# Performance work log

Measured on AMD Instinct MI355X. Metric: run time of the kernel, lower is better.

Reference implementation:

```python
import jax, jax.numpy as jnp
import numpy as np

EMB = 128
N_LEFT = 100000
N_RIGHT = 100000
N_EDGES = 600000
EDGE_FEAT = 1


def _ortho(key, shape):
    a = jax.random.normal(key, shape, dtype=jnp.float32)
    q, r = jnp.linalg.qr(a if shape[0] >= shape[1] else a.T)
    q = q * jnp.sign(jnp.diag(r))
    return q if shape[0] >= shape[1] else q.T


def setup_inputs() -> dict:
    key = jax.random.key(0)
    ks = jax.random.split(key, 12)
    return {
        "left_features": jax.random.normal(ks[0], (N_LEFT, EMB), dtype=jnp.float32),
        "edge_indices": jax.random.randint(ks[1], (2, N_EDGES), 0, N_LEFT, dtype=jnp.int32).astype(jnp.int64),
        "edge_features": jax.random.normal(ks[2], (N_EDGES, EDGE_FEAT), dtype=jnp.float32),
        "right_features": jax.random.normal(ks[3], (N_RIGHT, EMB), dtype=jnp.float32),
        "scatter_out_size": N_RIGHT,
        # parameters (orthogonal weights, zero biases, unit PreNorm scales)
        "W_left": _ortho(ks[4], (EMB, EMB)),
        "b_left": jnp.zeros((EMB,), jnp.float32),
        "W_edge": _ortho(ks[5], (EMB, EDGE_FEAT)),
        "W_right": _ortho(ks[6], (EMB, EMB)),
        "scale_final": jnp.ones((1,), jnp.float32),
        "W_final": _ortho(ks[7], (EMB, EMB)),
        "b_final": jnp.zeros((EMB,), jnp.float32),
        "scale_post": jnp.ones((1,), jnp.float32),
        "W_out1": _ortho(ks[8], (EMB, 2 * EMB)),
        "b_out1": jnp.zeros((EMB,), jnp.float32),
        "W_out2": _ortho(ks[9], (EMB, EMB)),
        "b_out2": jnp.zeros((EMB,), jnp.float32),
    }


def reference(left_features, edge_indices, edge_features, right_features,
              scatter_out_size, W_left, b_left, W_edge, W_right,
              scale_final, W_final, b_final, scale_post,
              W_out1, b_out1, W_out2, b_out2):
    # node / edge projections
    left_proj = left_features @ W_left.T + b_left            # [n_left, emb]
    edge_proj = edge_features @ W_edge.T                     # [n_edges, emb]
    right_proj = right_features @ W_right.T                  # [n_right, emb]
    # gather per-edge messages and combine
    joint = left_proj[edge_indices[0]] + edge_proj + right_proj[edge_indices[1]]
    # feature_module_final: PreNorm(scale only) -> ReLU -> Linear
    joint = jax.nn.relu(joint * scale_final) @ W_final.T + b_final
    # scatter-add onto right-side nodes (right_to_left=False)
    conv = jax.ops.segment_sum(joint, edge_indices[1], num_segments=scatter_out_size)
    conv = conv * scale_post
    # output MLP on [conv ; prev_right]
    h = jnp.concatenate([conv, right_features], axis=1)      # [n_right, 2*emb]
    h = jax.nn.relu(h @ W_out1.T + b_out1)
    return h @ W_out2.T + b_out2
```

## Files before the change

kernel.cpp:

```cpp
#include <hip/hip_runtime.h>

#define EMB 128

typedef __attribute__((ext_vector_type(8))) short short8;
typedef __attribute__((ext_vector_type(4))) short short4v;
typedef __attribute__((ext_vector_type(4))) float floatx4;

#define MFMA(a, b, c) __builtin_amdgcn_mfma_f32_16x16x32_bf16((a), (b), (c), 0, 0, 0)

__device__ __forceinline__ ushort f2b(float f) {
    unsigned u = __float_as_uint(f);
    return (ushort)((u + 0x7fff + ((u >> 16) & 1)) >> 16);
}
__device__ __forceinline__ float b2f(ushort h) {
    return __uint_as_float(((unsigned)h) << 16);
}
__device__ __forceinline__ short8 cvt8(const float* p) {
    float4 f0 = *(const float4*)p;
    float4 f1 = *(const float4*)(p + 4);
    short8 v;
    v[0] = f2b(f0.x); v[1] = f2b(f0.y); v[2] = f2b(f0.z); v[3] = f2b(f0.w);
    v[4] = f2b(f1.x); v[5] = f2b(f1.y); v[6] = f2b(f1.z); v[7] = f2b(f1.w);
    return v;
}

template <int RSH>
__device__ __forceinline__ void stage32k(const ushort* __restrict__ g,
                                         ushort* __restrict__ lds, int t) {
#pragma unroll
    for (int i = 0; i < 8; i++) {
        int a = i * 4096 + t * 16;
        short8 v = *(const short8*)(g + (a >> 1));
        int d = a ^ (((a >> RSH) & 7) << 4);
        *(short8*)((char*)lds + d) = v;
    }
}
__device__ __forceinline__ short8 ldsW8(const ushort* lds, int byte) {
    return *(const short8*)((const char*)lds + (byte ^ (((byte >> 8) & 7) << 4)));
}
__device__ __forceinline__ short8 ldsW9(const ushort* lds, int byte) {
    return *(const short8*)((const char*)lds + (byte ^ (((byte >> 9) & 7) << 4)));
}

__global__ __launch_bounds__(256) void k_cvthist(const float* __restrict__ w0,
                                                 const float* __restrict__ w1,
                                                 const float* __restrict__ w2,
                                                 const float* __restrict__ w3,
                                                 const float* __restrict__ w4,
                                                 ushort* __restrict__ dst,
                                                 const int* __restrict__ eidx,
                                                 int* __restrict__ cnt,
                                                 int n_edges) {
    int bid = blockIdx.x;
    if (bid < 384) {
        int i = bid * 256 + threadIdx.x;
        const float* src; int off;
        if (i < 16384)      { src = w0; off = i; }
        else if (i < 32768) { src = w1; off = i - 16384; }
        else if (i < 49152) { src = w2; off = i - 32768; }
        else if (i < 81920) { src = w3; off = i - 49152; }
        else                { src = w4; off = i - 81920; }
        dst[i] = f2b(src[off]);
    } else {
        int e = (bid - 384) * 256 + threadIdx.x;
        if (e < n_edges) atomicAdd(&cnt[eidx[n_edges + e]], 1);
    }
}

#define SCAN_CHUNK 4096
__global__ __launch_bounds__(1024) void k_scan1(const int* __restrict__ cnt,
                                                int* __restrict__ offs,
                                                int* __restrict__ bsum, int n) {
    __shared__ int buf[1024];
    int t = threadIdx.x;
    int i0 = blockIdx.x * SCAN_CHUNK + t * 4;
    int v[4];
#pragma unroll
    for (int u = 0; u < 4; u++) { int i = i0 + u; v[u] = (i < n) ? cnt[i] : 0; }
    int s = v[0] + v[1] + v[2] + v[3];
    buf[t] = s;
    __syncthreads();
    for (int d = 1; d < 1024; d <<= 1) {
        int x = (t >= d) ? buf[t - d] : 0;
        __syncthreads();
        buf[t] += x;
        __syncthreads();
    }
    int excl = buf[t] - s;
#pragma unroll
    for (int u = 0; u < 4; u++) { int i = i0 + u; if (i < n) offs[i] = excl; excl += v[u]; }
    if (t == 1023) bsum[blockIdx.x] = buf[1023];
}

__global__ __launch_bounds__(1024) void k_scan2(const int* __restrict__ bsum,
                                                int* __restrict__ offs,
                                                int* __restrict__ cursor, int n) {
    int bid = blockIdx.x;
    int base = 0;
    for (int j = 0; j < bid; j++) base += bsum[j];
    int i0 = bid * SCAN_CHUNK + threadIdx.x * 4;
#pragma unroll
    for (int u = 0; u < 4; u++) {
        int i = i0 + u;
        if (i < n) { int o = offs[i] + base; offs[i] = o; cursor[i] = o; }
    }
}

#define PROJ_PB 512
__global__ __launch_bounds__(256) void k_permproj(const int* __restrict__ eidx,
                                                  const float* __restrict__ ef,
                                                  int* __restrict__ cursor,
                                                  int2* __restrict__ sle,
                                                  int n_edges,
                                                  const float* __restrict__ XL,
                                                  const float* __restrict__ XR,
                                                  const ushort* __restrict__ WLb,
                                                  const ushort* __restrict__ WRb,
                                                  const float* __restrict__ bias,
                                                  ushort* __restrict__ YL,
                                                  ushort* __restrict__ YR,
                                                  int n, int eb) {
    __shared__ ushort Wlds[16384];
    int bid = blockIdx.x;
    if (bid < eb) {
        int e = bid * 256 + threadIdx.x;
        if (e < n_edges) {
            int r = eidx[n_edges + e];
            int p = atomicAdd(&cursor[r], 1);
            int2 v; v.x = eidx[e]; v.y = __float_as_int(ef[e]);
            sle[p] = v;
        }
        return;
    }
    bid -= eb;
    const float* X; const ushort* Wb; ushort* Y; int has_bias;
    if (bid < PROJ_PB) { X = XL; Wb = WLb; Y = YL; has_bias = 1; }
    else               { X = XR; Wb = WRb; Y = YR; has_bias = 0; bid -= PROJ_PB; }

    int t = threadIdx.x, wave = t >> 6, lane = t & 63;
    int m = lane & 15, quad = lane >> 4;

    stage32k<8>(Wb, Wlds, t);
    __syncthreads();

    int ntiles = (n + 127) >> 7;
    for (int tile = bid; tile < ntiles; tile += PROJ_PB) {
        size_t base = (size_t)tile * 128 + wave * 32;
        size_t ra = base + m;
        size_t rb = base + 16 + m;
        bool oka = ra < (size_t)n, okb = rb < (size_t)n;
        size_t rac = oka ? ra : (size_t)(n - 1);
        size_t rbc = okb ? rb : (size_t)(n - 1);
        const float* pa = X + rac * EMB;
        const float* pb = X + rbc * EMB;
        short8 xa[4], xb[4];
#pragma unroll
        for (int ks = 0; ks < 4; ks++) {
            xa[ks] = cvt8(pa + ks * 32 + quad * 8);
            xb[ks] = cvt8(pb + ks * 32 + quad * 8);
        }
#pragma unroll
        for (int wt = 0; wt < 8; wt++) {
            floatx4 a0 = {0.f, 0.f, 0.f, 0.f}, a1 = {0.f, 0.f, 0.f, 0.f};
#pragma unroll
            for (int ks = 0; ks < 4; ks++) {
                short8 w = ldsW8(Wlds, ((wt * 16 + m) << 8) + (ks << 6) + (quad << 4));
                a0 = MFMA(w, xa[ks], a0);
                a1 = MFMA(w, xb[ks], a1);
            }
            float b0 = 0.f, b1_ = 0.f, b2_ = 0.f, b3 = 0.f;
            if (has_bias) {
                float4 bb = *(const float4*)(bias + wt * 16 + quad * 4);
                b0 = bb.x; b1_ = bb.y; b2_ = bb.z; b3 = bb.w;
            }
            if (oka) {
                short4v o;
                o[0] = f2b(a0[0] + b0);
                o[1] = f2b(a0[1] + b1_);
                o[2] = f2b(a0[2] + b2_);
                o[3] = f2b(a0[3] + b3);
                *(short4v*)(Y + ra * EMB + wt * 16 + quad * 4) = o;
            }
            if (okb) {
                short4v o;
                o[0] = f2b(a1[0] + b0);
                o[1] = f2b(a1[1] + b1_);
                o[2] = f2b(a1[2] + b2_);
                o[3] = f2b(a1[3] + b3);
                *(short4v*)(Y + rb * EMB + wt * 16 + quad * 4) = o;
            }
        }
    }
}

__global__ __launch_bounds__(256) void k_reduce(const ushort* __restrict__ Pl,
                                                const ushort* __restrict__ Pr,
                                                const int2* __restrict__ sle,
                                                const float* __restrict__ We,
                                                const int* __restrict__ offs,
                                                const float* __restrict__ scale_final,
                                                ushort* __restrict__ S,
                                                int n_right, int n_edges) {
    int r = blockIdx.x * 4 + (threadIdx.x >> 6);
    if (r >= n_right) return;
    int lane = threadIdx.x & 63;
    int g = lane >> 4;
    int m = lane & 15;
    float scale = scale_final[0];

    float4 w0 = *(const float4*)(We + m * 8);
    float4 w1 = *(const float4*)(We + m * 8 + 4);
    short8 prv = *(const short8*)(Pr + (size_t)r * EMB + m * 8);
    float we[8], pr[8];
    we[0] = w0.x; we[1] = w0.y; we[2] = w0.z; we[3] = w0.w;
    we[4] = w1.x; we[5] = w1.y; we[6] = w1.z; we[7] = w1.w;
#pragma unroll
    for (int j = 0; j < 8; j++) pr[j] = b2f((ushort)prv[j]);

    float acc[8] = {0.f, 0.f, 0.f, 0.f, 0.f, 0.f, 0.f, 0.f};
    int s0 = offs[r];
    int s1 = (r + 1 < n_right) ? offs[r + 1] : n_edges;
    int e = s0 + g;
    for (; e + 4 < s1; e += 8) {
        int2 ea = sle[e];
        int2 eb = sle[e + 4];
        short8 pa = *(const short8*)(Pl + (size_t)ea.x * EMB + m * 8);
        short8 pb = *(const short8*)(Pl + (size_t)eb.x * EMB + m * 8);
        float fa = __int_as_float(ea.y), fb = __int_as_float(eb.y);
#pragma unroll
        for (int j = 0; j < 8; j++) {
            acc[j] += fmaxf((b2f((ushort)pa[j]) + pr[j] + fa * we[j]) * scale, 0.f);
            acc[j] += fmaxf((b2f((ushort)pb[j]) + pr[j] + fb * we[j]) * scale, 0.f);
        }
    }
    if (e < s1) {
        int2 ea = sle[e];
        short8 pa = *(const short8*)(Pl + (size_t)ea.x * EMB + m * 8);
        float fa = __int_as_float(ea.y);
#pragma unroll
        for (int j = 0; j < 8; j++)
            acc[j] += fmaxf((b2f((ushort)pa[j]) + pr[j] + fa * we[j]) * scale, 0.f);
    }
#pragma unroll
    for (int j = 0; j < 8; j++) {
        acc[j] += __shfl_xor(acc[j], 16);
        acc[j] += __shfl_xor(acc[j], 32);
    }
    if (g == 0) {
        short8 o;
#pragma unroll
        for (int j = 0; j < 8; j++) o[j] = f2b(acc[j]);
        *(short8*)(S + (size_t)r * EMB + m * 8) = o;
    }
}

__global__ __launch_bounds__(256) void k_out(const ushort* __restrict__ S,
                                             const float* __restrict__ right,
                                             const ushort* __restrict__ Wfb,
                                             const float* __restrict__ bf,
                                             const int* __restrict__ deg,
                                             const float* __restrict__ sc_post,
                                             const ushort* __restrict__ W1b,
                                             const float* __restrict__ b1,
                                             const ushort* __restrict__ W2b,
                                             const float* __restrict__ b2,
                                             float* __restrict__ out, int n) {
    __shared__ ushort Wlds[16384];
    __shared__ ushort H[64][136];
    __shared__ float degs[64];
    int t = threadIdx.x, wave = t >> 6, lane = t & 63;
    int m = lane & 15, quad = lane >> 4;
    size_t row0 = (size_t)blockIdx.x * 64;
    int rl = wave * 16 + m;
    size_t xrow = row0 + rl;
    size_t xrowc = (xrow < (size_t)n) ? xrow : (size_t)(n - 1);
    bool ok = (xrow < (size_t)n);
    float sp = sc_post[0];

    short8 s4[4], ar[4];
    const ushort* sr = S + xrowc * EMB;
    const float* rr = right + xrowc * EMB;
#pragma unroll
    for (int ks = 0; ks < 4; ks++)
        s4[ks] = *(const short8*)(sr + ks * 32 + quad * 8);
    stage32k<8>(Wfb, Wlds, t);
#pragma unroll
    for (int ks = 0; ks < 4; ks++)
        ar[ks] = cvt8(rr + ks * 32 + quad * 8);
    if (t < 64) {
        size_t rr2 = row0 + t;
        degs[t] = (rr2 < (size_t)n) ? (float)deg[rr2] : 0.f;
    }
    __syncthreads();
    float dd = degs[rl];

#pragma unroll
    for (int wt = 0; wt < 8; wt++) {
        floatx4 acc = {0.f, 0.f, 0.f, 0.f};
#pragma unroll
        for (int ks = 0; ks < 4; ks++) {
            short8 w = ldsW8(Wlds, ((wt * 16 + m) << 8) + (ks << 6) + (quad << 4));
            acc = MFMA(w, s4[ks], acc);
        }
        float4 bb = *(const float4*)(bf + wt * 16 + quad * 4);
        short4v o;
        o[0] = f2b((acc[0] + dd * bb.x) * sp);
        o[1] = f2b((acc[1] + dd * bb.y) * sp);
        o[2] = f2b((acc[2] + dd * bb.z) * sp);
        o[3] = f2b((acc[3] + dd * bb.w) * sp);
        *(short4v*)(&H[rl][wt * 16 + quad * 4]) = o;
    }
    short8 c4[4];
#pragma unroll
    for (int ks = 0; ks < 4; ks++)
        c4[ks] = *(const short8*)(&H[rl][ks * 32 + quad * 8]);
    __syncthreads();
    stage32k<9>(W1b, Wlds, t);
    __syncthreads();

#pragma unroll
    for (int wt = 0; wt < 4; wt++) {
        floatx4 acc = {0.f, 0.f, 0.f, 0.f};
        int rb = wt * 16 + m;
#pragma unroll
        for (int ks = 0; ks < 4; ks++) {
            short8 w = ldsW9(Wlds, (rb << 9) + (ks << 6) + (quad << 4));
            acc = MFMA(w, c4[ks], acc);
        }
#pragma unroll
        for (int ks = 0; ks < 4; ks++) {
            short8 w = ldsW9(Wlds, (rb << 9) + 256 + (ks << 6) + (quad << 4));
            acc = MFMA(w, ar[ks], acc);
        }
        float4 bb = *(const float4*)(b1 + wt * 16 + quad * 4);
        short4v o;
        o[0] = f2b(fmaxf(acc[0] + bb.x, 0.f));
        o[1] = f2b(fmaxf(acc[1] + bb.y, 0.f));
        o[2] = f2b(fmaxf(acc[2] + bb.z, 0.f));
        o[3] = f2b(fmaxf(acc[3] + bb.w, 0.f));
        *(short4v*)(&H[rl][wt * 16 + quad * 4]) = o;
    }
    __syncthreads();
    stage32k<9>(W1b + 16384, Wlds, t);
    __syncthreads();

#pragma unroll
    for (int wt = 4; wt < 8; wt++) {
        floatx4 acc = {0.f, 0.f, 0.f, 0.f};
        int rb = (wt - 4) * 16 + m;
#pragma unroll
        for (int ks = 0; ks < 4; ks++) {
            short8 w = ldsW9(Wlds, (rb << 9) + (ks << 6) + (quad << 4));
            acc = MFMA(w, c4[ks], acc);
        }
#pragma unroll
        for (int ks = 0; ks < 4; ks++) {
            short8 w = ldsW9(Wlds, (rb << 9) + 256 + (ks << 6) + (quad << 4));
            acc = MFMA(w, ar[ks], acc);
        }
        float4 bb = *(const float4*)(b1 + wt * 16 + quad * 4);
        short4v o;
        o[0] = f2b(fmaxf(acc[0] + bb.x, 0.f));
        o[1] = f2b(fmaxf(acc[1] + bb.y, 0.f));
        o[2] = f2b(fmaxf(acc[2] + bb.z, 0.f));
        o[3] = f2b(fmaxf(acc[3] + bb.w, 0.f));
        *(short4v*)(&H[rl][wt * 16 + quad * 4]) = o;
    }
    short8 h4[4];
#pragma unroll
    for (int ks = 0; ks < 4; ks++)
        h4[ks] = *(const short8*)(&H[rl][ks * 32 + quad * 8]);
    __syncthreads();
    stage32k<8>(W2b, Wlds, t);
    __syncthreads();

#pragma unroll
    for (int wt = 0; wt < 8; wt++) {
        floatx4 acc = {0.f, 0.f, 0.f, 0.f};
#pragma unroll
        for (int ks = 0; ks < 4; ks++) {
            short8 w = ldsW8(Wlds, ((wt * 16 + m) << 8) + (ks << 6) + (quad << 4));
            acc = MFMA(w, h4[ks], acc);
        }
        if (ok) {
            float4 bb = *(const float4*)(b2 + wt * 16 + quad * 4);
            float4 o;
            o.x = acc[0] + bb.x;
            o.y = acc[1] + bb.y;
            o.z = acc[2] + bb.z;
            o.w = acc[3] + bb.w;
            *(float4*)(out + xrow * EMB + wt * 16 + quad * 4) = o;
        }
    }
}

extern "C" void kernel_launch(void* const* d_in, const int* in_sizes, int n_in,
                              void* d_out, int out_size, void* d_ws, size_t ws_size,
                              hipStream_t stream) {
    const float* left   = (const float*)d_in[0];
    const int*   eidx   = (const int*)  d_in[1];
    const float* efeat  = (const float*)d_in[2];
    const float* right  = (const float*)d_in[3];
    const float* W_left = (const float*)d_in[5];
    const float* b_left = (const float*)d_in[6];
    const float* W_edge = (const float*)d_in[7];
    const float* W_right= (const float*)d_in[8];
    const float* sc_fin = (const float*)d_in[9];
    const float* W_fin  = (const float*)d_in[10];
    const float* b_fin  = (const float*)d_in[11];
    const float* sc_post= (const float*)d_in[12];
    const float* W_out1 = (const float*)d_in[13];
    const float* b_out1 = (const float*)d_in[14];
    const float* W_out2 = (const float*)d_in[15];
    const float* b_out2 = (const float*)d_in[16];

    int n_left  = in_sizes[0] / EMB;
    int n_edges = in_sizes[2];
    int n_right = in_sizes[3] / EMB;

    ushort* us = (ushort*)d_ws;
    ushort* Wl_b = us;
    ushort* Wr_b = us + 16384;
    ushort* Wf_b = us + 32768;
    ushort* W1_b = us + 49152;
    ushort* W2_b = us + 81920;
    ushort* Pl   = us + 98304;
    ushort* Pr   = Pl + (size_t)n_left * EMB;
    ushort* S    = Pr + (size_t)n_right * EMB;
    int* cnt    = (int*)(S + (size_t)n_right * EMB);
    int* offs   = cnt + n_right;
    int* cursor = offs + n_right;
    int* bsum   = cursor + n_right;
    int2* sle   = (int2*)(bsum + 64);

    hipMemsetAsync(cnt, 0, (size_t)n_right * sizeof(int), stream);

    int eb = (n_edges + 255) / 256;
    int nsb = (n_right + SCAN_CHUNK - 1) / SCAN_CHUNK;

    k_cvthist<<<384 + eb, 256, 0, stream>>>(W_left, W_right, W_fin, W_out1,
                                            W_out2, us, eidx, cnt, n_edges);

    k_scan1<<<nsb, 1024, 0, stream>>>(cnt, offs, bsum, n_right);
    k_scan2<<<nsb, 1024, 0, stream>>>(bsum, offs, cursor, n_right);

    k_permproj<<<eb + 2 * PROJ_PB, 256, 0, stream>>>(eidx, efeat, cursor, sle,
                                                     n_edges, left, right,
                                                     Wl_b, Wr_b, b_left,
                                                     Pl, Pr, n_left, eb);

    k_reduce<<<(n_right + 3) / 4, 256, 0, stream>>>(Pl, Pr, sle, W_edge, offs,
                                                    sc_fin, S, n_right, n_edges);

    k_out<<<(n_right + 63) / 64, 256, 0, stream>>>(S, right, Wf_b, b_fin,
                                                   cnt, sc_post, W1_b, b_out1,
                                                   W2_b, b_out2,
                                                   (float*)d_out, n_right);
}
```

Measured before the change: 346.3 us.

## Use one projection tile per block, overlap X loads with W staging, batch edge permutation

```diff
diff --git a/kernel.cpp b/kernel.cpp
--- a/kernel.cpp
+++ b/kernel.cpp
@@ -106,7 +106,6 @@
     }
 }
 
-#define PROJ_PB 512
 __global__ __launch_bounds__(256) void k_permproj(const int* __restrict__ eidx,
                                                   const float* __restrict__ ef,
                                                   int* __restrict__ cursor,
@@ -119,76 +118,88 @@
                                                   const float* __restrict__ bias,
                                                   ushort* __restrict__ YL,
                                                   ushort* __restrict__ YR,
-                                                  int n, int eb) {
+                                                  int n, int nblk) {
     __shared__ ushort Wlds[16384];
     int bid = blockIdx.x;
-    if (bid < eb) {
-        int e = bid * 256 + threadIdx.x;
-        if (e < n_edges) {
-            int r = eidx[n_edges + e];
-            int p = atomicAdd(&cursor[r], 1);
-            int2 v; v.x = eidx[e]; v.y = __float_as_int(ef[e]);
+    int t = threadIdx.x;
+
+    if (bid >= 2 * nblk) {
+        int e0 = (bid - 2 * nblk) * 512 + t;
+        int e1 = e0 + 256;
+        bool v0 = e0 < n_edges, v1 = e1 < n_edges;
+        int r0 = v0 ? eidx[n_edges + e0] : 0;
+        int r1 = v1 ? eidx[n_edges + e1] : 0;
+        int l0 = v0 ? eidx[e0] : 0;
+        int l1 = v1 ? eidx[e1] : 0;
+        float f0 = v0 ? ef[e0] : 0.f;
+        float f1 = v1 ? ef[e1] : 0.f;
+        if (v0) {
+            int p = atomicAdd(&cursor[r0], 1);
+            int2 v; v.x = l0; v.y = __float_as_int(f0);
             sle[p] = v;
         }
+        if (v1) {
+            int p = atomicAdd(&cursor[r1], 1);
+            int2 v; v.x = l1; v.y = __float_as_int(f1);
+            sle[p] = v;
+        }
         return;
     }
-    bid -= eb;
+
     const float* X; const ushort* Wb; ushort* Y; int has_bias;
-    if (bid < PROJ_PB) { X = XL; Wb = WLb; Y = YL; has_bias = 1; }
-    else               { X = XR; Wb = WRb; Y = YR; has_bias = 0; bid -= PROJ_PB; }
-
-    int t = threadIdx.x, wave = t >> 6, lane = t & 63;
+    if (bid < nblk) { X = XL; Wb = WLb; Y = YL; has_bias = 1; }
+    else            { X = XR; Wb = WRb; Y = YR; has_bias = 0; bid -= nblk; }
+
+    int wave = t >> 6, lane = t & 63;
     int m = lane & 15, quad = lane >> 4;
 
     stage32k<8>(Wb, Wlds, t);
-    __syncthreads();
-
-    int ntiles = (n + 127) >> 7;
-    for (int tile = bid; tile < ntiles; tile += PROJ_PB) {
-        size_t base = (size_t)tile * 128 + wave * 32;
-        size_t ra = base + m;
-        size_t rb = base + 16 + m;
-        bool oka = ra < (size_t)n, okb = rb < (size_t)n;
-        size_t rac = oka ? ra : (size_t)(n - 1);
-        size_t rbc = okb ? rb : (size_t)(n - 1);
-        const float* pa = X + rac * EMB;
-        const float* pb = X + rbc * EMB;
-        short8 xa[4], xb[4];
-#pragma unroll
-        for (int ks = 0; ks < 4; ks++) {
-            xa[ks] = cvt8(pa + ks * 32 + quad * 8);
-            xb[ks] = cvt8(pb + ks * 32 + quad * 8);
-        }
-#pragma unroll
-        for (int wt = 0; wt < 8; wt++) {
-            floatx4 a0 = {0.f, 0.f, 0.f, 0.f}, a1 = {0.f, 0.f, 0.f, 0.f};
-#pragma unroll
-            for (int ks = 0; ks < 4; ks++) {
-                short8 w = ldsW8(Wlds, ((wt * 16 + m) << 8) + (ks << 6) + (quad << 4));
-                a0 = MFMA(w, xa[ks], a0);
-                a1 = MFMA(w, xb[ks], a1);
-            }
-            float b0 = 0.f, b1_ = 0.f, b2_ = 0.f, b3 = 0.f;
-            if (has_bias) {
-                float4 bb = *(const float4*)(bias + wt * 16 + quad * 4);
-                b0 = bb.x; b1_ = bb.y; b2_ = bb.z; b3 = bb.w;
-            }
-            if (oka) {
-                short4v o;
-                o[0] = f2b(a0[0] + b0);
-                o[1] = f2b(a0[1] + b1_);
-                o[2] = f2b(a0[2] + b2_);
-                o[3] = f2b(a0[3] + b3);
-                *(short4v*)(Y + ra * EMB + wt * 16 + quad * 4) = o;
-            }
-            if (okb) {
-                short4v o;
-                o[0] = f2b(a1[0] + b0);
-                o[1] = f2b(a1[1] + b1_);
-                o[2] = f2b(a1[2] + b2_);
-                o[3] = f2b(a1[3] + b3);
-                *(short4v*)(Y + rb * EMB + wt * 16 + quad * 4) = o;
-            }
+
+    size_t base = (size_t)bid * 128 + wave * 32;
+    size_t ra = base + m;
+    size_t rb = base + 16 + m;
+    bool oka = ra < (size_t)n, okb = rb < (size_t)n;
+    size_t rac = oka ? ra : (size_t)(n - 1);
+    size_t rbc = okb ? rb : (size_t)(n - 1);
+    const float* pa = X + rac * EMB;
+    const float* pb = X + rbc * EMB;
+    short8 xa[4], xb[4];
+#pragma unroll
+    for (int ks = 0; ks < 4; ks++) {
+        xa[ks] = cvt8(pa + ks * 32 + quad * 8);
+        xb[ks] = cvt8(pb + ks * 32 + quad * 8);
+    }
+    __syncthreads();
+
+#pragma unroll
+    for (int wt = 0; wt < 8; wt++) {
+        floatx4 a0 = {0.f, 0.f, 0.f, 0.f}, a1 = {0.f, 0.f, 0.f, 0.f};
+#pragma unroll
+        for (int ks = 0; ks < 4; ks++) {
+            short8 w = ldsW8(Wlds, ((wt * 16 + m) << 8) + (ks << 6) + (quad << 4));
+            a0 = MFMA(w, xa[ks], a0);
+            a1 = MFMA(w, xb[ks], a1);
+        }
+        float b0 = 0.f, b1_ = 0.f, b2_ = 0.f, b3 = 0.f;
+        if (has_bias) {
+            float4 bb = *(const float4*)(bias + wt * 16 + quad * 4);
+            b0 = bb.x; b1_ = bb.y; b2_ = bb.z; b3 = bb.w;
+        }
+        if (oka) {
+            short4v o;
+            o[0] = f2b(a0[0] + b0);
+            o[1] = f2b(a0[1] + b1_);
+            o[2] = f2b(a0[2] + b2_);
+            o[3] = f2b(a0[3] + b3);
+            *(short4v*)(Y + ra * EMB + wt * 16 + quad * 4) = o;
+        }
+        if (okb) {
+            short4v o;
+            o[0] = f2b(a1[0] + b0);
+            o[1] = f2b(a1[1] + b1_);
+            o[2] = f2b(a1[2] + b2_);
+            o[3] = f2b(a1[3] + b3);
+            *(short4v*)(Y + rb * EMB + wt * 16 + quad * 4) = o;
         }
     }
 }
@@ -435,19 +446,21 @@
 
     hipMemsetAsync(cnt, 0, (size_t)n_right * sizeof(int), stream);
 
-    int eb = (n_edges + 255) / 256;
+    int ebh = (n_edges + 255) / 256;
+    int ebs = (n_edges + 511) / 512;
+    int nblk = (n_left + 127) / 128;
     int nsb = (n_right + SCAN_CHUNK - 1) / SCAN_CHUNK;
 
-    k_cvthist<<<384 + eb, 256, 0, stream>>>(W_left, W_right, W_fin, W_out1,
-                                            W_out2, us, eidx, cnt, n_edges);
+    k_cvthist<<<384 + ebh, 256, 0, stream>>>(W_left, W_right, W_fin, W_out1,
+                                             W_out2, us, eidx, cnt, n_edges);
 
     k_scan1<<<nsb, 1024, 0, stream>>>(cnt, offs, bsum, n_right);
     k_scan2<<<nsb, 1024, 0, stream>>>(bsum, offs, cursor, n_right);
 
-    k_permproj<<<eb + 2 * PROJ_PB, 256, 0, stream>>>(eidx, efeat, cursor, sle,
-                                                     n_edges, left, right,
-                                                     Wl_b, Wr_b, b_left,
-                                                     Pl, Pr, n_left, eb);
+    k_permproj<<<2 * nblk + ebs, 256, 0, stream>>>(eidx, efeat, cursor, sle,
+                                                   n_edges, left, right,
+                                                   Wl_b, Wr_b, b_left,
+                                                   Pl, Pr, n_left, nblk);
 
     k_reduce<<<(n_right + 3) / 4, 256, 0, stream>>>(Pl, Pr, sle, W_edge, offs,
                                                     sc_fin, S, n_right, n_edges);
```

Measured after the change: 355.2 us. +2.6%, slower.
